# Optimization experiments

Hardware: AMD Instinct MI355X
Metric: run time of the kernel (lower is better)

Reference implementation:

```python
import jax, jax.numpy as jnp
import numpy as np

EPS = 1e-5

def layernorm(t, gamma, beta):
    mu = jnp.mean(t, axis=-1, keepdims=True)
    var = jnp.mean(jnp.square(t - mu), axis=-1, keepdims=True)
    return (t - mu) * jax.lax.rsqrt(var + EPS) * gamma + beta

def setup_inputs() -> dict:
    key = jax.random.key(0)
    ks = jax.random.split(key, 9)
    B, M, N, C, D = 4, 4096, 32, 256, 128
    x = jax.random.normal(ks[0], (B, M, C), dtype=jnp.float32)
    y = jax.random.normal(ks[1], (B, M, N, C), dtype=jnp.float32)
    z = jax.random.normal(ks[2], (B, M, N, 1), dtype=jnp.float32)
    s = 1.0 / np.sqrt(C)
    Wq = jax.random.normal(ks[3], (C, D), dtype=jnp.float32) * s
    bq = jnp.zeros((D,), dtype=jnp.float32)
    Wk = jax.random.normal(ks[4], (C, D), dtype=jnp.float32) * s
    bk = jnp.zeros((D,), dtype=jnp.float32)
    q_gamma = jnp.ones((C,), dtype=jnp.float32)
    q_beta = jnp.zeros((C,), dtype=jnp.float32)
    k_gamma = jnp.ones((C,), dtype=jnp.float32)
    k_beta = jnp.zeros((C,), dtype=jnp.float32)
    return {"x": x, "y": y, "z": z, "q_gamma": q_gamma, "q_beta": q_beta,
            "Wq": Wq, "bq": bq, "k_gamma": k_gamma, "k_beta": k_beta,
            "Wk": Wk, "bk": bk}

def reference(x, y, z, q_gamma, q_beta, Wq, bq, k_gamma, k_beta, Wk, bk):
    D = Wq.shape[1]
    scale = D ** (-0.5)
    q = layernorm(x, q_gamma, q_beta) @ Wq + bq          # (B, M, D)
    k = layernorm(y, k_gamma, k_beta) @ Wk + bk          # (B, M, N, D)
    # single query vs N keys per node: (B, M, N)
    dot = scale * jnp.einsum('bmd,bmnd->bmn', q, k)
    attn = jax.nn.softmax(dot, axis=-1)[..., None]       # (B, M, N, 1)
    a = jnp.sum(attn * z, axis=-2)                       # (B, M, 1)
    return a
```

## Files before the change

### kernel.cpp

```cpp
#include <hip/hip_runtime.h>
#include <math.h>

#define NROWS 16384
#define NN 32
#define NC 256
#define ND 128
#define RB 8
#define LNEPS 1e-5f
#define SCALE 0.08838834764831845f

typedef float vfloat4 __attribute__((ext_vector_type(4)));

#define OFF_MT   0
#define OFF_UVEC 65536
#define OFF_VV   65792
#define OFF_M1   66048
#define OFF_WG   66304
#define OFF_SCAL 66560

__device__ __forceinline__ float red16(float v) {
    int t;
    t = __builtin_amdgcn_update_dpp(0, __float_as_int(v), 0x121, 0xf, 0xf, false);
    v += __int_as_float(t);
    t = __builtin_amdgcn_update_dpp(0, __float_as_int(v), 0x122, 0xf, 0xf, false);
    v += __int_as_float(t);
    t = __builtin_amdgcn_update_dpp(0, __float_as_int(v), 0x124, 0xf, 0xf, false);
    v += __int_as_float(t);
    t = __builtin_amdgcn_update_dpp(0, __float_as_int(v), 0x128, 0xf, 0xf, false);
    v += __int_as_float(t);
    return v;
}

__global__ __launch_bounds__(256)
void ca_prep_a(const float* __restrict__ Wq, const float* __restrict__ Wk,
               const float* __restrict__ qg, const float* __restrict__ qb,
               const float* __restrict__ kg, float* __restrict__ ws) {
    __shared__ __align__(16) float wkrow[ND];
    __shared__ float red[8];
    const int j = blockIdx.x;
    const int c = threadIdx.x;
    const int lane = c & 63, wv = c >> 6;
    if (c < ND / 4) *(float4*)(wkrow + 4 * c) = *(const float4*)(Wk + j * ND + 4 * c);
    __syncthreads();
    float m = 0.f;
    #pragma unroll 8
    for (int d = 0; d < ND; d += 4) {
        const float4 wq4 = *(const float4*)(Wq + c * ND + d);
        const float4 wk4 = *(const float4*)(wkrow + d);
        m += wq4.x * wk4.x + wq4.y * wk4.y + wq4.z * wk4.z + wq4.w * wk4.w;
    }
    const float kgj = kg[j];
    const float mpp = kgj * qg[c] * m;
    ws[OFF_MT + c * NC + j] = mpp;
    float a = red16(mpp), b = red16(kgj * m * qb[c]);
    a += __shfl_xor(a, 16, 64); b += __shfl_xor(b, 16, 64);
    a += __shfl_xor(a, 32, 64); b += __shfl_xor(b, 32, 64);
    if (lane == 0) { red[wv] = a; red[4 + wv] = b; }
    __syncthreads();
    if (c == 0) {
        ws[OFF_UVEC + j] = red[0] + red[1] + red[2] + red[3];
        ws[OFF_VV + j]   = red[4] + red[5] + red[6] + red[7];
    }
}

__global__ __launch_bounds__(256)
void ca_prep_b(const float* __restrict__ Wq, const float* __restrict__ Wk,
               const float* __restrict__ qg, const float* __restrict__ qb,
               const float* __restrict__ kg, const float* __restrict__ kb,
               const float* __restrict__ bq, const float* __restrict__ bk,
               float* __restrict__ ws) {
    __shared__ float h[ND];
    __shared__ float htmp[2][ND];
    __shared__ float red[16];
    const int t = threadIdx.x, lane = t & 63, wv = t >> 6;
    {
        float s = 0.f;
        const float* mrow = ws + OFF_MT + t * NC;
        #pragma unroll 8
        for (int j2 = 0; j2 < NC; j2 += 4) {
            const float4 m4 = *(const float4*)(mrow + j2);
            s += (m4.x + m4.y) + (m4.z + m4.w);
        }
        ws[OFF_M1 + t] = s;
    }
    {
        const int d = t & (ND - 1), half = t >> 7;
        float s = 0.f;
        #pragma unroll 8
        for (int j = half * 128; j < half * 128 + 128; ++j) s += Wk[j * ND + d] * kb[j];
        htmp[half][d] = s;
    }
    __syncthreads();
    if (t < ND) h[t] = bk[t] + htmp[0][t] + htmp[1][t];
    __syncthreads();
    float vvj;
    {
        float s = 0.f;
        #pragma unroll 8
        for (int d = 0; d < ND; d += 4) {
            const float4 w4 = *(const float4*)(Wk + t * ND + d);
            const float4 b4 = *(const float4*)(bq + d);
            s += w4.x * b4.x + w4.y * b4.y + w4.z * b4.z + w4.w * b4.w;
        }
        vvj = ws[OFF_VV + t] + kg[t] * s;
        ws[OFF_VV + t] = vvj;
    }
    float w = 0.f;
    #pragma unroll 8
    for (int d = 0; d < ND; d += 4) {
        const float4 w4 = *(const float4*)(Wq + t * ND + d);
        w += w4.x * h[d] + w4.y * h[d + 1] + w4.z * h[d + 2] + w4.w * h[d + 3];
    }
    ws[OFF_WG + t] = qg[t] * w;
    float r0 = qg[t] * w;
    float r1 = qb[t] * w + ((t < ND) ? bq[t] * h[t] : 0.f);
    float r2 = ws[OFF_UVEC + t];
    float r3 = vvj;
    r0 = red16(r0); r1 = red16(r1); r2 = red16(r2); r3 = red16(r3);
    #pragma unroll
    for (int s = 16; s < 64; s <<= 1) {
        r0 += __shfl_xor(r0, s, 64); r1 += __shfl_xor(r1, s, 64);
        r2 += __shfl_xor(r2, s, 64); r3 += __shfl_xor(r3, s, 64);
    }
    if (lane == 0) { red[wv] = r0; red[4 + wv] = r1; red[8 + wv] = r2; red[12 + wv] = r3; }
    __syncthreads();
    if (t == 0) {
        ws[OFF_SCAL + 0] = red[0] + red[1] + red[2] + red[3];
        ws[OFF_SCAL + 1] = red[4] + red[5] + red[6] + red[7];
        ws[OFF_SCAL + 2] = red[8] + red[9] + red[10] + red[11];
        ws[OFF_SCAL + 3] = red[12] + red[13] + red[14] + red[15];
    }
}

__global__ __launch_bounds__(256, 4)
void ca_main(const float* __restrict__ x, const float* __restrict__ y,
             const float* __restrict__ z, const float* __restrict__ ws,
             float* __restrict__ out) {
    __shared__ __align__(16) float xs[RB * NC];
    __shared__ __align__(16) float tp[4 * RB * NC];
    const int tid = threadIdx.x;
    const int lane = tid & 63;
    const int wv = tid >> 6;
    const int row0 = blockIdx.x * RB;

    float mu_[2], rstd_[2], cst_[2], sgr_[2];

    {
        const float4 wg4 = *(const float4*)(ws + OFF_WG + 4 * lane);
        const float4 m14 = *(const float4*)(ws + OFF_M1 + 4 * lane);
        const float s0 = ws[OFF_SCAL + 0], s1c = ws[OFF_SCAL + 1];
        const float s2c = ws[OFF_SCAL + 2], s3c = ws[OFF_SCAL + 3];
        #pragma unroll
        for (int jj = 0; jj < 2; ++jj) {
            const int r = 2 * wv + jj;
            const float4 x4 = *(const float4*)(x + (size_t)(row0 + r) * NC + 4 * lane);
            *(float4*)(xs + r * NC + 4 * lane) = x4;
            float a = (x4.x + x4.y) + (x4.z + x4.w);
            float b = x4.x * x4.x + x4.y * x4.y + x4.z * x4.z + x4.w * x4.w;
            float cw = x4.x * wg4.x + x4.y * wg4.y + x4.z * wg4.z + x4.w * wg4.w;
            float dm = x4.x * m14.x + x4.y * m14.y + x4.z * m14.z + x4.w * m14.w;
            a = red16(a); b = red16(b); cw = red16(cw); dm = red16(dm);
            #pragma unroll
            for (int s = 16; s < 64; s <<= 1) {
                a += __shfl_xor(a, s, 64); b += __shfl_xor(b, s, 64);
                cw += __shfl_xor(cw, s, 64); dm += __shfl_xor(dm, s, 64);
            }
            const float mu = a * (1.f / NC);
            const float var = b * (1.f / NC) - mu * mu;
            const float rstd = rsqrtf(var + LNEPS);
            mu_[jj] = mu; rstd_[jj] = rstd;
            cst_[jj] = rstd * (cw - mu * s0) + s1c;
            sgr_[jj] = rstd * (dm - mu * s2c) + s3c;
        }
    }
    __syncthreads();

    {
        float acc[RB][4];
        #pragma unroll
        for (int r = 0; r < RB; ++r) { acc[r][0] = acc[r][1] = acc[r][2] = acc[r][3] = 0.f; }
        const float* Mt = ws + OFF_MT;
        const int cb = 64 * wv;
        #pragma unroll 2
        for (int cc = 0; cc < 64; cc += 4) {
            const int c = cb + cc;
            const float4 m0  = *(const float4*)(Mt + (c + 0) * NC + 4 * lane);
            const float4 m1v = *(const float4*)(Mt + (c + 1) * NC + 4 * lane);
            const float4 m2  = *(const float4*)(Mt + (c + 2) * NC + 4 * lane);
            const float4 m3  = *(const float4*)(Mt + (c + 3) * NC + 4 * lane);
            #pragma unroll
            for (int r = 0; r < RB; ++r) {
                const float4 xv = *(const float4*)(xs + r * NC + c);
                acc[r][0] = fmaf(xv.x, m0.x, fmaf(xv.y, m1v.x, fmaf(xv.z, m2.x, fmaf(xv.w, m3.x, acc[r][0]))));
                acc[r][1] = fmaf(xv.x, m0.y, fmaf(xv.y, m1v.y, fmaf(xv.z, m2.y, fmaf(xv.w, m3.y, acc[r][1]))));
                acc[r][2] = fmaf(xv.x, m0.z, fmaf(xv.y, m1v.z, fmaf(xv.z, m2.z, fmaf(xv.w, m3.z, acc[r][2]))));
                acc[r][3] = fmaf(xv.x, m0.w, fmaf(xv.y, m1v.w, fmaf(xv.z, m2.w, fmaf(xv.w, m3.w, acc[r][3]))));
            }
        }
        #pragma unroll
        for (int r = 0; r < RB; ++r) {
            float4 o; o.x = acc[r][0]; o.y = acc[r][1]; o.z = acc[r][2]; o.w = acc[r][3];
            *(float4*)(tp + (wv * RB + r) * NC + 4 * lane) = o;
        }
    }
    __syncthreads();

    {
        const float4 u4 = *(const float4*)(ws + OFF_UVEC + 4 * lane);
        const float4 v4 = *(const float4*)(ws + OFF_VV + 4 * lane);
        #pragma unroll
        for (int jj = 0; jj < 2; ++jj) {
            const int r = 2 * wv + jj;
            const float4 t0 = *(const float4*)(tp + (0 * RB + r) * NC + 4 * lane);
            const float4 t1 = *(const float4*)(tp + (1 * RB + r) * NC + 4 * lane);
            const float4 t2 = *(const float4*)(tp + (2 * RB + r) * NC + 4 * lane);
            const float4 t3 = *(const float4*)(tp + (3 * RB + r) * NC + 4 * lane);
            const float rstd = rstd_[jj], mu = mu_[jj];
            float4 gp;
            gp.x = rstd * ((t0.x + t1.x + t2.x + t3.x) - mu * u4.x) + v4.x;
            gp.y = rstd * ((t0.y + t1.y + t2.y + t3.y) - mu * u4.y) + v4.y;
            gp.z = rstd * ((t0.z + t1.z + t2.z + t3.z) - mu * u4.z) + v4.z;
            gp.w = rstd * ((t0.w + t1.w + t2.w + t3.w) - mu * u4.w) + v4.w;
            *(float4*)(tp + r * NC + 4 * lane) = gp;
        }
    }

    {
        const int g = lane >> 4;
        const int i = lane & 15;
        const int sig = 8 * g + (lane & 7);
        #pragma unroll 1
        for (int jj = 0; jj < 2; ++jj) {
            const int r = 2 * wv + jj;
            const size_t row = (size_t)row0 + r;
            const float* gl = tp + r * NC + 4 * i;
            const vfloat4 g0 = *(const vfloat4*)(gl + 0);
            const vfloat4 g1 = *(const vfloat4*)(gl + 64);
            const vfloat4 g2 = *(const vfloat4*)(gl + 128);
            const vfloat4 g3 = *(const vfloat4*)(gl + 192);
            const float cst = cst_[jj], sg = sgr_[jj];
            const float* kb0 = y + row * (size_t)(NN * NC) + (8 * g) * NC + 4 * i;
            const float zv = z[row * NN + sig];
            float dv = 0.f;
            vfloat4 ya0, yb0, yc0, yd0, ya1, yb1, yc1, yd1;
            vfloat4 ya2, yb2, yc2, yd2, ya3, yb3, yc3, yd3;

#define LOADS(S, K) \
            ya##S = *(const vfloat4*)(kb0 + (K) * NC + 0); \
            yb##S = *(const vfloat4*)(kb0 + (K) * NC + 64); \
            yc##S = *(const vfloat4*)(kb0 + (K) * NC + 128); \
            yd##S = *(const vfloat4*)(kb0 + (K) * NC + 192);

#define REDK(S, K) { \
            float s1 = (((ya##S.x + ya##S.y) + (ya##S.z + ya##S.w)) + ((yb##S.x + yb##S.y) + (yb##S.z + yb##S.w))) \
                     + (((yc##S.x + yc##S.y) + (yc##S.z + yc##S.w)) + ((yd##S.x + yd##S.y) + (yd##S.z + yd##S.w))); \
            float s2 = ya##S.x*ya##S.x + ya##S.y*ya##S.y + ya##S.z*ya##S.z + ya##S.w*ya##S.w \
                     + yb##S.x*yb##S.x + yb##S.y*yb##S.y + yb##S.z*yb##S.z + yb##S.w*yb##S.w \
                     + yc##S.x*yc##S.x + yc##S.y*yc##S.y + yc##S.z*yc##S.z + yc##S.w*yc##S.w \
                     + yd##S.x*yd##S.x + yd##S.y*yd##S.y + yd##S.z*yd##S.z + yd##S.w*yd##S.w; \
            float s3 = ya##S.x*g0.x + ya##S.y*g0.y + ya##S.z*g0.z + ya##S.w*g0.w \
                     + yb##S.x*g1.x + yb##S.y*g1.y + yb##S.z*g1.z + yb##S.w*g1.w \
                     + yc##S.x*g2.x + yc##S.y*g2.y + yc##S.z*g2.z + yc##S.w*g2.w \
                     + yd##S.x*g3.x + yd##S.y*g3.y + yd##S.z*g3.z + yd##S.w*g3.w; \
            s1 = red16(s1); s2 = red16(s2); s3 = red16(s3); \
            const float mun = s1 * (1.f / NC); \
            const float varn = s2 * (1.f / NC) - mun * mun; \
            const float rsd = rsqrtf(varn + LNEPS); \
            const float dt = SCALE * (rsd * (s3 - mun * sg) + cst); \
            dv = ((lane & 7) == (K)) ? dt : dv; }

            LOADS(0, 0) LOADS(1, 1) LOADS(2, 2) LOADS(3, 3)
            REDK(0, 0) LOADS(0, 4)
            REDK(1, 1) LOADS(1, 5)
            REDK(2, 2) LOADS(2, 6)
            REDK(3, 3) LOADS(3, 7)
            REDK(0, 4) REDK(1, 5) REDK(2, 6) REDK(3, 7)
#undef LOADS
#undef REDK

            float mx = dv;
            mx = fmaxf(mx, __shfl_xor(mx, 1, 64));
            mx = fmaxf(mx, __shfl_xor(mx, 2, 64));
            mx = fmaxf(mx, __shfl_xor(mx, 4, 64));
            mx = fmaxf(mx, __shfl_xor(mx, 16, 64));
            mx = fmaxf(mx, __shfl_xor(mx, 32, 64));
            const float e = __expf(dv - mx);
            float num = e * zv, den = e;
            num += __shfl_xor(num, 1, 64);  den += __shfl_xor(den, 1, 64);
            num += __shfl_xor(num, 2, 64);  den += __shfl_xor(den, 2, 64);
            num += __shfl_xor(num, 4, 64);  den += __shfl_xor(den, 4, 64);
            num += __shfl_xor(num, 16, 64); den += __shfl_xor(den, 16, 64);
            num += __shfl_xor(num, 32, 64); den += __shfl_xor(den, 32, 64);
            if (lane == 0) out[row] = num / den;
        }
    }
}

extern "C" void kernel_launch(void* const* d_in, const int* in_sizes, int n_in,
                              void* d_out, int out_size, void* d_ws, size_t ws_size,
                              hipStream_t stream) {
    const float* x  = (const float*)d_in[0];
    const float* y  = (const float*)d_in[1];
    const float* z  = (const float*)d_in[2];
    const float* qg = (const float*)d_in[3];
    const float* qb = (const float*)d_in[4];
    const float* Wq = (const float*)d_in[5];
    const float* bq = (const float*)d_in[6];
    const float* kg = (const float*)d_in[7];
    const float* kb = (const float*)d_in[8];
    const float* Wk = (const float*)d_in[9];
    const float* bk = (const float*)d_in[10];
    float* out = (float*)d_out;
    float* ws = (float*)d_ws;

    ca_prep_a<<<NC, 256, 0, stream>>>(Wq, Wk, qg, qb, kg, ws);
    ca_prep_b<<<1, 256, 0, stream>>>(Wq, Wk, qg, qb, kg, kb, bq, bk, ws);
    ca_main<<<NROWS / RB, 256, 0, stream>>>(x, y, z, ws, out);
}
```

Measured before the change: 150.0 us.

## Halve rows per block and remap y-streaming to 32 lanes per key

Reduces rows per block from 8 to 4 so each wave owns one row, and raises launch bounds to 8 blocks per CU for more occupancy. The key-streaming loop is remapped: each key row is now spread across 32 lanes (two float4 loads each) with 16 keys per half-wave, instead of 16 lanes and four loads per key. This shrinks live registers and shared memory per block to allow more waves to hide memory latency on the dominant y read. The cost is an extra cross-lane shuffle per key reduction, and the projection GEMM over the transposed matrix is amortized over fewer rows per block.

```diff
diff --git a/kernel.cpp b/kernel.cpp
--- a/kernel.cpp
+++ b/kernel.cpp
@@ -5,7 +5,7 @@
 #define NN 32
 #define NC 256
 #define ND 128
-#define RB 8
+#define RB 4
 #define LNEPS 1e-5f
 #define SCALE 0.08838834764831845f
 
@@ -132,7 +132,7 @@
     }
 }
 
-__global__ __launch_bounds__(256, 4)
+__global__ __launch_bounds__(256, 8)
 void ca_main(const float* __restrict__ x, const float* __restrict__ y,
              const float* __restrict__ z, const float* __restrict__ ws,
              float* __restrict__ out) {
@@ -143,35 +143,30 @@
     const int wv = tid >> 6;
     const int row0 = blockIdx.x * RB;
 
-    float mu_[2], rstd_[2], cst_[2], sgr_[2];
+    float mu_r, rstd_r, cst_r, sg_r;
 
     {
         const float4 wg4 = *(const float4*)(ws + OFF_WG + 4 * lane);
         const float4 m14 = *(const float4*)(ws + OFF_M1 + 4 * lane);
         const float s0 = ws[OFF_SCAL + 0], s1c = ws[OFF_SCAL + 1];
         const float s2c = ws[OFF_SCAL + 2], s3c = ws[OFF_SCAL + 3];
+        const float4 x4 = *(const float4*)(x + (size_t)(row0 + wv) * NC + 4 * lane);
+        *(float4*)(xs + wv * NC + 4 * lane) = x4;
+        float a = (x4.x + x4.y) + (x4.z + x4.w);
+        float b = x4.x * x4.x + x4.y * x4.y + x4.z * x4.z + x4.w * x4.w;
+        float cw = x4.x * wg4.x + x4.y * wg4.y + x4.z * wg4.z + x4.w * wg4.w;
+        float dm = x4.x * m14.x + x4.y * m14.y + x4.z * m14.z + x4.w * m14.w;
+        a = red16(a); b = red16(b); cw = red16(cw); dm = red16(dm);
         #pragma unroll
-        for (int jj = 0; jj < 2; ++jj) {
-            const int r = 2 * wv + jj;
-            const float4 x4 = *(const float4*)(x + (size_t)(row0 + r) * NC + 4 * lane);
-            *(float4*)(xs + r * NC + 4 * lane) = x4;
-            float a = (x4.x + x4.y) + (x4.z + x4.w);
-            float b = x4.x * x4.x + x4.y * x4.y + x4.z * x4.z + x4.w * x4.w;
-            float cw = x4.x * wg4.x + x4.y * wg4.y + x4.z * wg4.z + x4.w * wg4.w;
-            float dm = x4.x * m14.x + x4.y * m14.y + x4.z * m14.z + x4.w * m14.w;
-            a = red16(a); b = red16(b); cw = red16(cw); dm = red16(dm);
-            #pragma unroll
-            for (int s = 16; s < 64; s <<= 1) {
-                a += __shfl_xor(a, s, 64); b += __shfl_xor(b, s, 64);
-                cw += __shfl_xor(cw, s, 64); dm += __shfl_xor(dm, s, 64);
-            }
-            const float mu = a * (1.f / NC);
-            const float var = b * (1.f / NC) - mu * mu;
-            const float rstd = rsqrtf(var + LNEPS);
-            mu_[jj] = mu; rstd_[jj] = rstd;
-            cst_[jj] = rstd * (cw - mu * s0) + s1c;
-            sgr_[jj] = rstd * (dm - mu * s2c) + s3c;
-        }
+        for (int s = 16; s < 64; s <<= 1) {
+            a += __shfl_xor(a, s, 64); b += __shfl_xor(b, s, 64);
+            cw += __shfl_xor(cw, s, 64); dm += __shfl_xor(dm, s, 64);
+        }
+        mu_r = a * (1.f / NC);
+        const float var = b * (1.f / NC) - mu_r * mu_r;
+        rstd_r = rsqrtf(var + LNEPS);
+        cst_r = rstd_r * (cw - mu_r * s0) + s1c;
+        sg_r  = rstd_r * (dm - mu_r * s2c) + s3c;
     }
     __syncthreads();
 
@@ -208,91 +203,85 @@
     {
         const float4 u4 = *(const float4*)(ws + OFF_UVEC + 4 * lane);
         const float4 v4 = *(const float4*)(ws + OFF_VV + 4 * lane);
-        #pragma unroll
-        for (int jj = 0; jj < 2; ++jj) {
-            const int r = 2 * wv + jj;
-            const float4 t0 = *(const float4*)(tp + (0 * RB + r) * NC + 4 * lane);
-            const float4 t1 = *(const float4*)(tp + (1 * RB + r) * NC + 4 * lane);
-            const float4 t2 = *(const float4*)(tp + (2 * RB + r) * NC + 4 * lane);
-            const float4 t3 = *(const float4*)(tp + (3 * RB + r) * NC + 4 * lane);
-            const float rstd = rstd_[jj], mu = mu_[jj];
-            float4 gp;
-            gp.x = rstd * ((t0.x + t1.x + t2.x + t3.x) - mu * u4.x) + v4.x;
-            gp.y = rstd * ((t0.y + t1.y + t2.y + t3.y) - mu * u4.y) + v4.y;
-            gp.z = rstd * ((t0.z + t1.z + t2.z + t3.z) - mu * u4.z) + v4.z;
-            gp.w = rstd * ((t0.w + t1.w + t2.w + t3.w) - mu * u4.w) + v4.w;
-            *(float4*)(tp + r * NC + 4 * lane) = gp;
-        }
-    }
-
-    {
-        const int g = lane >> 4;
-        const int i = lane & 15;
-        const int sig = 8 * g + (lane & 7);
-        #pragma unroll 1
-        for (int jj = 0; jj < 2; ++jj) {
-            const int r = 2 * wv + jj;
-            const size_t row = (size_t)row0 + r;
-            const float* gl = tp + r * NC + 4 * i;
-            const vfloat4 g0 = *(const vfloat4*)(gl + 0);
-            const vfloat4 g1 = *(const vfloat4*)(gl + 64);
-            const vfloat4 g2 = *(const vfloat4*)(gl + 128);
-            const vfloat4 g3 = *(const vfloat4*)(gl + 192);
-            const float cst = cst_[jj], sg = sgr_[jj];
-            const float* kb0 = y + row * (size_t)(NN * NC) + (8 * g) * NC + 4 * i;
-            const float zv = z[row * NN + sig];
-            float dv = 0.f;
-            vfloat4 ya0, yb0, yc0, yd0, ya1, yb1, yc1, yd1;
-            vfloat4 ya2, yb2, yc2, yd2, ya3, yb3, yc3, yd3;
-
-#define LOADS(S, K) \
-            ya##S = *(const vfloat4*)(kb0 + (K) * NC + 0); \
-            yb##S = *(const vfloat4*)(kb0 + (K) * NC + 64); \
-            yc##S = *(const vfloat4*)(kb0 + (K) * NC + 128); \
-            yd##S = *(const vfloat4*)(kb0 + (K) * NC + 192);
-
-#define REDK(S, K) { \
-            float s1 = (((ya##S.x + ya##S.y) + (ya##S.z + ya##S.w)) + ((yb##S.x + yb##S.y) + (yb##S.z + yb##S.w))) \
-                     + (((yc##S.x + yc##S.y) + (yc##S.z + yc##S.w)) + ((yd##S.x + yd##S.y) + (yd##S.z + yd##S.w))); \
-            float s2 = ya##S.x*ya##S.x + ya##S.y*ya##S.y + ya##S.z*ya##S.z + ya##S.w*ya##S.w \
-                     + yb##S.x*yb##S.x + yb##S.y*yb##S.y + yb##S.z*yb##S.z + yb##S.w*yb##S.w \
-                     + yc##S.x*yc##S.x + yc##S.y*yc##S.y + yc##S.z*yc##S.z + yc##S.w*yc##S.w \
-                     + yd##S.x*yd##S.x + yd##S.y*yd##S.y + yd##S.z*yd##S.z + yd##S.w*yd##S.w; \
-            float s3 = ya##S.x*g0.x + ya##S.y*g0.y + ya##S.z*g0.z + ya##S.w*g0.w \
-                     + yb##S.x*g1.x + yb##S.y*g1.y + yb##S.z*g1.z + yb##S.w*g1.w \
-                     + yc##S.x*g2.x + yc##S.y*g2.y + yc##S.z*g2.z + yc##S.w*g2.w \
-                     + yd##S.x*g3.x + yd##S.y*g3.y + yd##S.z*g3.z + yd##S.w*g3.w; \
-            s1 = red16(s1); s2 = red16(s2); s3 = red16(s3); \
-            const float mun = s1 * (1.f / NC); \
-            const float varn = s2 * (1.f / NC) - mun * mun; \
-            const float rsd = rsqrtf(varn + LNEPS); \
-            const float dt = SCALE * (rsd * (s3 - mun * sg) + cst); \
-            dv = ((lane & 7) == (K)) ? dt : dv; }
-
-            LOADS(0, 0) LOADS(1, 1) LOADS(2, 2) LOADS(3, 3)
-            REDK(0, 0) LOADS(0, 4)
-            REDK(1, 1) LOADS(1, 5)
-            REDK(2, 2) LOADS(2, 6)
-            REDK(3, 3) LOADS(3, 7)
-            REDK(0, 4) REDK(1, 5) REDK(2, 6) REDK(3, 7)
+        const float4 t0 = *(const float4*)(tp + (0 * RB + wv) * NC + 4 * lane);
+        const float4 t1 = *(const float4*)(tp + (1 * RB + wv) * NC + 4 * lane);
+        const float4 t2 = *(const float4*)(tp + (2 * RB + wv) * NC + 4 * lane);
+        const float4 t3 = *(const float4*)(tp + (3 * RB + wv) * NC + 4 * lane);
+        float4 gp;
+        gp.x = rstd_r * ((t0.x + t1.x + t2.x + t3.x) - mu_r * u4.x) + v4.x;
+        gp.y = rstd_r * ((t0.y + t1.y + t2.y + t3.y) - mu_r * u4.y) + v4.y;
+        gp.z = rstd_r * ((t0.z + t1.z + t2.z + t3.z) - mu_r * u4.z) + v4.z;
+        gp.w = rstd_r * ((t0.w + t1.w + t2.w + t3.w) - mu_r * u4.w) + v4.w;
+        *(float4*)(xs + wv * NC + 4 * lane) = gp;
+    }
+
+    {
+        const int half = lane >> 5;
+        const int i = lane & 31;
+        const int sig = (lane & 15) + 16 * half;
+        const size_t row = (size_t)row0 + wv;
+        const float* gl = xs + wv * NC;
+        const vfloat4 gA = *(const vfloat4*)(gl + 4 * i);
+        const vfloat4 gB = *(const vfloat4*)(gl + 128 + 4 * i);
+        const float cst = cst_r, sg = sg_r;
+        const float* kb0 = y + row * (size_t)(NN * NC) + (16 * half) * NC + 4 * i;
+        const float zv = z[row * NN + sig];
+        float dv = 0.f;
+        vfloat4 a0, b0, a1, b1;
+
+#define LOADS(S, T) \
+        a##S = *(const vfloat4*)(kb0 + (T) * NC); \
+        b##S = *(const vfloat4*)(kb0 + (T) * NC + 128);
+
+#define REDK(S, T) { \
+        float s1 = ((a##S.x + a##S.y) + (a##S.z + a##S.w)) + ((b##S.x + b##S.y) + (b##S.z + b##S.w)); \
+        float s2 = a##S.x*a##S.x + a##S.y*a##S.y + a##S.z*a##S.z + a##S.w*a##S.w \
+                 + b##S.x*b##S.x + b##S.y*b##S.y + b##S.z*b##S.z + b##S.w*b##S.w; \
+        float s3 = a##S.x*gA.x + a##S.y*gA.y + a##S.z*gA.z + a##S.w*gA.w \
+                 + b##S.x*gB.x + b##S.y*gB.y + b##S.z*gB.z + b##S.w*gB.w; \
+        s1 = red16(s1); s2 = red16(s2); s3 = red16(s3); \
+        s1 += __shfl_xor(s1, 16, 64); \
+        s2 += __shfl_xor(s2, 16, 64); \
+        s3 += __shfl_xor(s3, 16, 64); \
+        const float mun = s1 * (1.f / NC); \
+        const float varn = s2 * (1.f / NC) - mun * mun; \
+        const float rsd = rsqrtf(varn + LNEPS); \
+        const float dt = SCALE * (rsd * (s3 - mun * sg) + cst); \
+        dv = ((lane & 15) == (T)) ? dt : dv; }
+
+        LOADS(0, 0) LOADS(1, 1)
+        REDK(0, 0)  LOADS(0, 2)
+        REDK(1, 1)  LOADS(1, 3)
+        REDK(0, 2)  LOADS(0, 4)
+        REDK(1, 3)  LOADS(1, 5)
+        REDK(0, 4)  LOADS(0, 6)
+        REDK(1, 5)  LOADS(1, 7)
+        REDK(0, 6)  LOADS(0, 8)
+        REDK(1, 7)  LOADS(1, 9)
+        REDK(0, 8)  LOADS(0, 10)
+        REDK(1, 9)  LOADS(1, 11)
+        REDK(0, 10) LOADS(0, 12)
+        REDK(1, 11) LOADS(1, 13)
+        REDK(0, 12) LOADS(0, 14)
+        REDK(1, 13) LOADS(1, 15)
+        REDK(0, 14) REDK(1, 15)
 #undef LOADS
 #undef REDK
 
-            float mx = dv;
-            mx = fmaxf(mx, __shfl_xor(mx, 1, 64));
-            mx = fmaxf(mx, __shfl_xor(mx, 2, 64));
-            mx = fmaxf(mx, __shfl_xor(mx, 4, 64));
-            mx = fmaxf(mx, __shfl_xor(mx, 16, 64));
-            mx = fmaxf(mx, __shfl_xor(mx, 32, 64));
-            const float e = __expf(dv - mx);
-            float num = e * zv, den = e;
-            num += __shfl_xor(num, 1, 64);  den += __shfl_xor(den, 1, 64);
-            num += __shfl_xor(num, 2, 64);  den += __shfl_xor(den, 2, 64);
-            num += __shfl_xor(num, 4, 64);  den += __shfl_xor(den, 4, 64);
-            num += __shfl_xor(num, 16, 64); den += __shfl_xor(den, 16, 64);
-            num += __shfl_xor(num, 32, 64); den += __shfl_xor(den, 32, 64);
-            if (lane == 0) out[row] = num / den;
-        }
+        float mx = dv;
+        mx = fmaxf(mx, __shfl_xor(mx, 1, 64));
+        mx = fmaxf(mx, __shfl_xor(mx, 2, 64));
+        mx = fmaxf(mx, __shfl_xor(mx, 4, 64));
+        mx = fmaxf(mx, __shfl_xor(mx, 8, 64));
+        mx = fmaxf(mx, __shfl_xor(mx, 32, 64));
+        const float e = __expf(dv - mx);
+        float num = e * zv, den = e;
+        num += __shfl_xor(num, 1, 64);  den += __shfl_xor(den, 1, 64);
+        num += __shfl_xor(num, 2, 64);  den += __shfl_xor(den, 2, 64);
+        num += __shfl_xor(num, 4, 64);  den += __shfl_xor(den, 4, 64);
+        num += __shfl_xor(num, 8, 64);  den += __shfl_xor(den, 8, 64);
+        num += __shfl_xor(num, 32, 64); den += __shfl_xor(den, 32, 64);
+        if (lane == 0) out[row] = num / den;
     }
 }
 
```

Measured after the change: 155.1 us. 3.4% more time.
